# Kernel optimization log

Hardware: AMD Instinct MI355X
Metric: run time of the kernel (lower is better)

Reference implementation:

```python
import jax, jax.numpy as jnp
import numpy as np

E, TOPK = 8, 2
N_EMBD, TEXT_DIM, FULL = 1024, 1024, 1024
BS, SEQ = 8, 512

def setup_inputs() -> dict:
    key = jax.random.key(0)
    ks = jax.random.split(key, 8)
    return {
        "x": jax.random.normal(ks[0], (BS, SEQ, N_EMBD), jnp.float32),
        "dec_embeddings": jax.random.normal(ks[1], (BS, TEXT_DIM), jnp.float32),
        # router is zero-init in the module, but use small random weights so top-k is non-degenerate
        "router_w": jax.random.normal(ks[2], (E, TEXT_DIM), jnp.float32) * 0.02,
        "router_b": jnp.zeros((E,), jnp.float32),
        "w1": jax.random.normal(ks[3], (E, N_EMBD, N_EMBD), jnp.float32) * 0.02,
        "w2": jax.random.normal(ks[4], (E, N_EMBD, FULL), jnp.float32) * 0.02,
        "b1": jnp.zeros((E, 1, N_EMBD), jnp.float32),
        "b2": jnp.zeros((E, 1, FULL), jnp.float32),
    }

def reference(x, dec_embeddings, router_w, router_b, w1, w2, b1, b2):
    bs, seqlen, n_embd = x.shape
    logits = dec_embeddings @ router_w.T + router_b          # (bs, E)
    gate_probs = jax.nn.softmax(logits, axis=-1)
    topk_w, topk_idx = jax.lax.top_k(gate_probs, TOPK)       # (bs, k)
    topk_w = topk_w / jnp.sum(topk_w, axis=-1, keepdims=True)
    # dense all-expert 2-layer MLP (as written in the original)
    hidden = jax.nn.relu(jnp.einsum('bsn,enh->ebsh', x, w1) + b1[:, None])   # (E,bs,S,H)
    out_all = jnp.einsum('ebsh,ehf->ebsf', hidden, w2) + b2[:, None]          # (E,bs,S,F)
    out_b = jnp.transpose(out_all, (1, 0, 2, 3))             # (bs,E,S,F)
    # gather top-k expert outputs per batch item and combine
    sel = jnp.take_along_axis(out_b, topk_idx[:, :, None, None], axis=1)      # (bs,k,S,F)
    final_output = jnp.sum(topk_w[:, :, None, None] * sel, axis=1)            # (bs,S,F)
    combined_mask = jnp.max(jax.nn.one_hot(topk_idx, E, dtype=x.dtype), axis=1)  # (bs,E)
    aux_loss = E * jnp.sum(jnp.mean(gate_probs, axis=0) * jnp.mean(combined_mask, axis=0))
    return final_output, aux_loss, combined_mask, logits
```

## Files before the change

### kernel.cpp

```cpp
#include <hip/hip_runtime.h>
#include <hip/hip_bf16.h>
#include <stdint.h>

#define EXP 8
#define DIM 1024
#define SEQL 512
#define BATCH 8
#define OUT_FINAL_N (BATCH * SEQL * DIM)
#define OFF_AUX    4194304
#define OFF_MASK   4194305
#define OFF_LOGITS 4194369

typedef __bf16 bf16_t;
typedef bf16_t bf16x8 __attribute__((ext_vector_type(8)));
typedef bf16_t bf16x4 __attribute__((ext_vector_type(4)));
typedef float  f32x4  __attribute__((ext_vector_type(4)));

typedef __attribute__((address_space(1))) void* as1p;
typedef __attribute__((address_space(3))) void* as3p;

__device__ __forceinline__ void glds16(const void* g, void* l) {
  __builtin_amdgcn_global_load_lds((as1p)(void*)g, (as3p)l, 16, 0, 0);
}

__global__ __launch_bounds__(256) void prep_kernel(
    const float* __restrict__ x, const float* __restrict__ dec,
    const float* __restrict__ rw, const float* __restrict__ rb,
    const float* __restrict__ w1, const float* __restrict__ w2,
    bf16_t* __restrict__ xb, bf16_t* __restrict__ w1t, bf16_t* __restrict__ w2t,
    float* __restrict__ out_aux, float* __restrict__ out_mask,
    float* __restrict__ out_logits, int* __restrict__ idx_ws,
    float* __restrict__ w_ws) {
  __shared__ float tile[64][129];
  __shared__ float part[256];
  __shared__ float lg64[64];
  __shared__ float probs[64];
  __shared__ float msk[64];
  const int bid = blockIdx.x;
  const int t = threadIdx.x;

  if (bid < 2048) {
    const int z = bid >> 7;
    const int rem = bid & 127;
    const int k0 = (rem >> 4) * 128;
    const int n0 = (rem & 15) * 64;
    const float* src = (z < 8) ? (w1 + (size_t)z * DIM * DIM)
                               : (w2 + (size_t)(z - 8) * DIM * DIM);
    bf16_t* dst = (z < 8) ? (w1t + (size_t)z * DIM * DIM)
                          : (w2t + (size_t)(z - 8) * DIM * DIM);
    const int rr = t >> 4, c4 = t & 15;
    float4 v[8];
#pragma unroll
    for (int i = 0; i < 8; ++i)
      v[i] = *(const float4*)(src + (size_t)(k0 + rr + 16 * i) * DIM + n0 + c4 * 4);
#pragma unroll
    for (int i = 0; i < 8; ++i) {
      const int k = rr + 16 * i;
      tile[c4 * 4 + 0][k] = v[i].x;
      tile[c4 * 4 + 1][k] = v[i].y;
      tile[c4 * 4 + 2][k] = v[i].z;
      tile[c4 * 4 + 3][k] = v[i].w;
    }
    __syncthreads();
#pragma unroll
    for (int ii = 0; ii < 4; ++ii) {
      const int n = (t >> 4) + 16 * ii;
      const int c = t & 15;
      bf16x8 o;
#pragma unroll
      for (int wd = 0; wd < 8; ++wd) o[wd] = (bf16_t)tile[n][c * 8 + wd];
      *(bf16x8*)(dst + (size_t)(n0 + n) * DIM + k0 + c * 8) = o;
    }
  } else if (bid < 2048 + 512) {
    const int i0 = (bid - 2048) * 2048 + t;
    float4 v[8];
#pragma unroll
    for (int i = 0; i < 8; ++i) v[i] = ((const float4*)x)[i0 + i * 256];
#pragma unroll
    for (int i = 0; i < 8; ++i) {
      bf16x4 o;
      o[0] = (bf16_t)v[i].x; o[1] = (bf16_t)v[i].y;
      o[2] = (bf16_t)v[i].z; o[3] = (bf16_t)v[i].w;
      ((bf16x4*)xb)[i0 + i * 256] = o;
    }
  } else {
    const int p = t >> 2, seg = t & 3;
    const int b = p >> 3, e = p & 7;
    const float4* dv = (const float4*)(dec + b * DIM + seg * 256);
    const float4* wv = (const float4*)(rw + e * DIM + seg * 256);
    float s = 0.f;
#pragma unroll 8
    for (int i = 0; i < 64; ++i) {
      float4 a = dv[i], c = wv[i];
      s += a.x * c.x + a.y * c.y + a.z * c.z + a.w * c.w;
    }
    part[t] = s;
    __syncthreads();
    if (seg == 0) {
      float l = part[t] + part[t + 1] + part[t + 2] + part[t + 3] + rb[e];
      lg64[p] = l;
      out_logits[p] = l;
    }
    __syncthreads();
    if (t < 8) {
      float l[8];
      float mx = -1e30f;
#pragma unroll
      for (int k = 0; k < 8; ++k) { l[k] = lg64[t * 8 + k]; mx = fmaxf(mx, l[k]); }
      float pe[8];
      float sum = 0.f;
#pragma unroll
      for (int k = 0; k < 8; ++k) { pe[k] = expf(l[k] - mx); sum += pe[k]; }
      float inv = 1.f / sum;
#pragma unroll
      for (int k = 0; k < 8; ++k) { pe[k] *= inv; probs[t * 8 + k] = pe[k]; }
      int i0 = 0;
#pragma unroll
      for (int k = 1; k < 8; ++k) if (pe[k] > pe[i0]) i0 = k;
      int i1 = (i0 == 0) ? 1 : 0;
#pragma unroll
      for (int k = 0; k < 8; ++k) if (k != i0 && pe[k] > pe[i1]) i1 = k;
      float p0 = pe[i0], p1 = pe[i1];
      float invs = 1.f / (p0 + p1);
      idx_ws[t * 2] = i0;
      idx_ws[t * 2 + 1] = i1;
      w_ws[t * 2] = p0 * invs;
      w_ws[t * 2 + 1] = p1 * invs;
#pragma unroll
      for (int k = 0; k < 8; ++k) {
        float m = (k == i0 || k == i1) ? 1.f : 0.f;
        msk[t * 8 + k] = m;
        out_mask[t * 8 + k] = m;
      }
    }
    __syncthreads();
    if (t == 0) {
      float aux = 0.f;
#pragma unroll
      for (int k = 0; k < 8; ++k) {
        float mp = 0.f, mm = 0.f;
#pragma unroll
        for (int bb = 0; bb < 8; ++bb) { mp += probs[bb * 8 + k]; mm += msk[bb * 8 + k]; }
        aux += (mp * 0.125f) * (mm * 0.125f);
      }
      out_aux[0] = 8.f * aux;
    }
  }
}

__device__ __forceinline__ void kloop_64x128(const bf16_t* __restrict__ A,
                                             const bf16_t* __restrict__ Bt,
                                             char* sA, char* sB, int t,
                                             f32x4 acc[2][4]) {
  const int lane = t & 63;
  const int w = t >> 6, wr = w >> 1, wc = w & 1;
  const int m15 = lane & 15, q = lane >> 4;
  const int rl = t >> 2, cp = (t & 3) ^ (rl & 3);
  const bf16_t* ga  = A  + (size_t)rl * DIM + cp * 8;
  const bf16_t* gb0 = Bt + (size_t)rl * DIM + cp * 8;
  const bf16_t* gb1 = gb0 + (size_t)64 * DIM;

  const char* ra[2];
  const char* rb[4];
#pragma unroll
  for (int i = 0; i < 2; ++i) {
    const int r = wr * 32 + i * 16 + m15;
    ra[i] = sA + r * 64 + ((q ^ (r & 3)) * 16);
  }
#pragma unroll
  for (int j = 0; j < 4; ++j) {
    const int n = wc * 64 + j * 16 + m15;
    rb[j] = sB + n * 64 + ((q ^ (n & 3)) * 16);
  }

  glds16(ga,  sA + t * 16);
  glds16(gb0, sB + t * 16);
  glds16(gb1, sB + 4096 + t * 16);

  for (int kt = 0; kt < 32; ++kt) {
    const int cur = kt & 1;
    __syncthreads();
    if (kt < 31) {
      const int nxt = cur ^ 1;
      const int off = (kt + 1) * 32;
      glds16(ga + off,  sA + nxt * 4096 + t * 16);
      glds16(gb0 + off, sB + nxt * 8192 + t * 16);
      glds16(gb1 + off, sB + nxt * 8192 + 4096 + t * 16);
    }
    bf16x8 af[2], bfr[4];
#pragma unroll
    for (int i = 0; i < 2; ++i) af[i] = *(const bf16x8*)(ra[i] + cur * 4096);
#pragma unroll
    for (int j = 0; j < 4; ++j) bfr[j] = *(const bf16x8*)(rb[j] + cur * 8192);
#pragma unroll
    for (int i = 0; i < 2; ++i)
#pragma unroll
      for (int j = 0; j < 4; ++j)
        acc[i][j] = __builtin_amdgcn_mfma_f32_16x16x32_bf16(af[i], bfr[j], acc[i][j], 0, 0, 0);
  }
}

__global__ __launch_bounds__(256, 4) void gemm1_kernel(const bf16_t* __restrict__ xb,
                                                       const bf16_t* __restrict__ w1t,
                                                       const float* __restrict__ b1,
                                                       const int* __restrict__ topk_idx,
                                                       bf16_t* __restrict__ hidden) {
  __shared__ __align__(16) char smem[24576];
  const int tid = threadIdx.x;
  const int bN = blockIdx.x, bM = blockIdx.y, slot = blockIdx.z;
  const int b = slot >> 1;
  const int e = topk_idx[slot];

  const bf16_t* A  = xb + ((size_t)b * SEQL + bM * 64) * DIM;
  const bf16_t* Bt = w1t + ((size_t)e * DIM + bN * 128) * DIM;

  f32x4 acc[2][4];
#pragma unroll
  for (int i = 0; i < 2; ++i)
#pragma unroll
    for (int j = 0; j < 4; ++j) acc[i][j] = {0.f, 0.f, 0.f, 0.f};

  kloop_64x128(A, Bt, smem, smem + 8192, tid, acc);

  __syncthreads();
  bf16_t* hb = (bf16_t*)smem;
  const int lane = tid & 63, w = tid >> 6;
  const int wr = w >> 1, wc = w & 1;
  const int m15 = lane & 15, q = lane >> 4;
  const float* be = b1 + e * DIM;
#pragma unroll
  for (int i = 0; i < 2; ++i)
#pragma unroll
    for (int j = 0; j < 4; ++j) {
      const int colL = wc * 64 + j * 16 + m15;
      const float bias = be[bN * 128 + colL];
#pragma unroll
      for (int r = 0; r < 4; ++r) {
        const int rowL = wr * 32 + i * 16 + q * 4 + r;
        hb[rowL * 136 + colL] = (bf16_t)fmaxf(acc[i][j][r] + bias, 0.f);
      }
    }
  __syncthreads();
  bf16_t* H = hidden + (size_t)slot * SEQL * DIM + ((size_t)bM * 64) * DIM + bN * 128;
#pragma unroll
  for (int ii = 0; ii < 4; ++ii) {
    const int r = (tid >> 4) + 16 * ii;
    const int c = tid & 15;
    bf16x8 vv = *(const bf16x8*)(hb + r * 136 + c * 8);
    *(bf16x8*)(H + (size_t)r * DIM + c * 8) = vv;
  }
}

__global__ __launch_bounds__(512, 4) void gemm2_kernel(const bf16_t* __restrict__ hidden,
                                                       const bf16_t* __restrict__ w2t,
                                                       const float* __restrict__ b2,
                                                       const int* __restrict__ topk_idx,
                                                       const float* __restrict__ topk_w,
                                                       float* __restrict__ out) {
  __shared__ __align__(16) char smem[49152];
  const int tid = threadIdx.x;
  const int g = tid >> 8;
  const int t = tid & 255;
  const int bN = blockIdx.x, bM = blockIdx.y, b = blockIdx.z;
  const int e = topk_idx[b * 2 + g];
  const float sg = topk_w[b * 2 + g];

  char* sA = smem + g * 24576;
  char* sB = smem + g * 24576 + 8192;

  f32x4 acc[2][4];
#pragma unroll
  for (int i = 0; i < 2; ++i)
#pragma unroll
    for (int j = 0; j < 4; ++j) acc[i][j] = {0.f, 0.f, 0.f, 0.f};

  const bf16_t* A  = hidden + ((size_t)(b * 2 + g) * SEQL + bM * 64) * DIM;
  const bf16_t* Bt = w2t + ((size_t)e * DIM + bN * 128) * DIM;
  kloop_64x128(A, Bt, sA, sB, t, acc);

  __syncthreads();
  float* scr = (float*)smem;
  const int lane = t & 63, wv = t >> 6;
  const int wr = wv >> 1, wc = wv & 1;
  const int m15 = lane & 15, q = lane >> 4;
  const float w0 = topk_w[b * 2], w1v = topk_w[b * 2 + 1];
  const float* be0 = b2 + topk_idx[b * 2] * DIM;
  const float* be1 = b2 + topk_idx[b * 2 + 1] * DIM;
  float* O = out + (size_t)b * SEQL * DIM;

#pragma unroll
  for (int half = 0; half < 2; ++half) {
    if (g == 1) {
#pragma unroll
      for (int j = 0; j < 4; ++j)
#pragma unroll
        for (int r = 0; r < 4; ++r)
          scr[(j * 4 + r) * 256 + t] = sg * acc[half][j][r];
    }
    __syncthreads();
    if (g == 0) {
#pragma unroll
      for (int j = 0; j < 4; ++j) {
        const int col = bN * 128 + wc * 64 + j * 16 + m15;
        const float bb = w0 * be0[col] + w1v * be1[col];
        const int row = bM * 64 + wr * 32 + half * 16 + q * 4;
#pragma unroll
        for (int r = 0; r < 4; ++r)
          O[(size_t)(row + r) * DIM + col] =
              sg * acc[half][j][r] + scr[(j * 4 + r) * 256 + t] + bb;
      }
    }
    __syncthreads();
  }
}

extern "C" void kernel_launch(void* const* d_in, const int* in_sizes, int n_in,
                              void* d_out, int out_size, void* d_ws, size_t ws_size,
                              hipStream_t stream) {
  const float* x   = (const float*)d_in[0];
  const float* dec = (const float*)d_in[1];
  const float* rw  = (const float*)d_in[2];
  const float* rb  = (const float*)d_in[3];
  const float* w1  = (const float*)d_in[4];
  const float* w2  = (const float*)d_in[5];
  const float* b1  = (const float*)d_in[6];
  const float* b2  = (const float*)d_in[7];
  float* out = (float*)d_out;

  char* ws = (char*)d_ws;
  bf16_t* xb   = (bf16_t*)(ws);
  bf16_t* w1t  = (bf16_t*)(ws + (8u << 20));
  bf16_t* w2t  = (bf16_t*)(ws + (24u << 20));
  bf16_t* hid  = (bf16_t*)(ws + (40u << 20));
  int*    idxw = (int*)(ws + (56u << 20));
  float*  ww   = (float*)(ws + (56u << 20) + 64);

  hipLaunchKernelGGL(prep_kernel, dim3(2048 + 512 + 1), dim3(256), 0, stream,
                     x, dec, rw, rb, w1, w2, xb, w1t, w2t,
                     out + OFF_AUX, out + OFF_MASK, out + OFF_LOGITS, idxw, ww);
  hipLaunchKernelGGL(gemm1_kernel, dim3(8, 8, 16), dim3(256), 0, stream,
                     xb, w1t, b1, idxw, hid);
  hipLaunchKernelGGL(gemm2_kernel, dim3(8, 8, 8), dim3(512), 0, stream,
                     hid, w2t, b2, idxw, ww, out);
}
```

Before: 203.3 us.

## Overlap w2 transpose/convert with gemm1 by interleaving blocks in one kernel

Moves the fp32→bf16 transpose of w2 out of the prep kernel and into the gemm1 launch, interleaving transpose blocks (even ids) with gemm1 tile blocks (odd ids). The goal is to hide the memory-bound w2 conversion behind the compute-bound first GEMM and shorten the prep kernel. In exchange, gemm1 loses its launch_bounds occupancy hint of 4 and now uses a larger shared buffer sized for the transpose tile, which may reduce gemm1 occupancy.

```diff
diff --git a/kernel.cpp b/kernel.cpp
--- a/kernel.cpp
+++ b/kernel.cpp
@@ -23,56 +23,54 @@
   __builtin_amdgcn_global_load_lds((as1p)(void*)g, (as3p)l, 16, 0, 0);
 }
 
-__global__ __launch_bounds__(256) void prep_kernel(
+__device__ __forceinline__ void transpose_tile(const float* __restrict__ src,
+                                               bf16_t* __restrict__ dst,
+                                               int k0, int n0, int t,
+                                               char* smem_) {
+  float (*tile)[129] = (float (*)[129])smem_;
+  const int rr = t >> 4, c4 = t & 15;
+  float4 v[8];
+#pragma unroll
+  for (int i = 0; i < 8; ++i)
+    v[i] = *(const float4*)(src + (size_t)(k0 + rr + 16 * i) * DIM + n0 + c4 * 4);
+#pragma unroll
+  for (int i = 0; i < 8; ++i) {
+    const int k = rr + 16 * i;
+    tile[c4 * 4 + 0][k] = v[i].x;
+    tile[c4 * 4 + 1][k] = v[i].y;
+    tile[c4 * 4 + 2][k] = v[i].z;
+    tile[c4 * 4 + 3][k] = v[i].w;
+  }
+  __syncthreads();
+#pragma unroll
+  for (int ii = 0; ii < 4; ++ii) {
+    const int n = (t >> 4) + 16 * ii;
+    const int c = t & 15;
+    bf16x8 o;
+#pragma unroll
+    for (int wd = 0; wd < 8; ++wd) o[wd] = (bf16_t)tile[n][c * 8 + wd];
+    *(bf16x8*)(dst + (size_t)(n0 + n) * DIM + k0 + c * 8) = o;
+  }
+}
+
+__global__ __launch_bounds__(256) void k1_prep(
     const float* __restrict__ x, const float* __restrict__ dec,
     const float* __restrict__ rw, const float* __restrict__ rb,
-    const float* __restrict__ w1, const float* __restrict__ w2,
-    bf16_t* __restrict__ xb, bf16_t* __restrict__ w1t, bf16_t* __restrict__ w2t,
+    const float* __restrict__ w1,
+    bf16_t* __restrict__ xb, bf16_t* __restrict__ w1t,
     float* __restrict__ out_aux, float* __restrict__ out_mask,
     float* __restrict__ out_logits, int* __restrict__ idx_ws,
     float* __restrict__ w_ws) {
-  __shared__ float tile[64][129];
-  __shared__ float part[256];
-  __shared__ float lg64[64];
-  __shared__ float probs[64];
-  __shared__ float msk[64];
+  __shared__ __align__(16) char smem[33024];
   const int bid = blockIdx.x;
   const int t = threadIdx.x;
 
-  if (bid < 2048) {
-    const int z = bid >> 7;
-    const int rem = bid & 127;
-    const int k0 = (rem >> 4) * 128;
-    const int n0 = (rem & 15) * 64;
-    const float* src = (z < 8) ? (w1 + (size_t)z * DIM * DIM)
-                               : (w2 + (size_t)(z - 8) * DIM * DIM);
-    bf16_t* dst = (z < 8) ? (w1t + (size_t)z * DIM * DIM)
-                          : (w2t + (size_t)(z - 8) * DIM * DIM);
-    const int rr = t >> 4, c4 = t & 15;
-    float4 v[8];
-#pragma unroll
-    for (int i = 0; i < 8; ++i)
-      v[i] = *(const float4*)(src + (size_t)(k0 + rr + 16 * i) * DIM + n0 + c4 * 4);
-#pragma unroll
-    for (int i = 0; i < 8; ++i) {
-      const int k = rr + 16 * i;
-      tile[c4 * 4 + 0][k] = v[i].x;
-      tile[c4 * 4 + 1][k] = v[i].y;
-      tile[c4 * 4 + 2][k] = v[i].z;
-      tile[c4 * 4 + 3][k] = v[i].w;
-    }
-    __syncthreads();
-#pragma unroll
-    for (int ii = 0; ii < 4; ++ii) {
-      const int n = (t >> 4) + 16 * ii;
-      const int c = t & 15;
-      bf16x8 o;
-#pragma unroll
-      for (int wd = 0; wd < 8; ++wd) o[wd] = (bf16_t)tile[n][c * 8 + wd];
-      *(bf16x8*)(dst + (size_t)(n0 + n) * DIM + k0 + c * 8) = o;
-    }
-  } else if (bid < 2048 + 512) {
-    const int i0 = (bid - 2048) * 2048 + t;
+  if (bid < 1024) {
+    const int z = bid >> 7, rem = bid & 127;
+    transpose_tile(w1 + (size_t)z * DIM * DIM, w1t + (size_t)z * DIM * DIM,
+                   (rem >> 4) * 128, (rem & 15) * 64, t, smem);
+  } else if (bid < 1024 + 512) {
+    const int i0 = (bid - 1024) * 2048 + t;
     float4 v[8];
 #pragma unroll
     for (int i = 0; i < 8; ++i) v[i] = ((const float4*)x)[i0 + i * 256];
@@ -84,6 +82,10 @@
       ((bf16x4*)xb)[i0 + i * 256] = o;
     }
   } else {
+    float* part = (float*)smem;
+    float* lg64 = part + 256;
+    float* probs = lg64 + 64;
+    float* msk = probs + 64;
     const int p = t >> 2, seg = t & 3;
     const int b = p >> 3, e = p & 7;
     const float4* dv = (const float4*)(dec + b * DIM + seg * 256);
@@ -200,14 +202,25 @@
   }
 }
 
-__global__ __launch_bounds__(256, 4) void gemm1_kernel(const bf16_t* __restrict__ xb,
-                                                       const bf16_t* __restrict__ w1t,
-                                                       const float* __restrict__ b1,
-                                                       const int* __restrict__ topk_idx,
-                                                       bf16_t* __restrict__ hidden) {
-  __shared__ __align__(16) char smem[24576];
+__global__ __launch_bounds__(256) void k2_w2t_gemm1(
+    const float* __restrict__ w2, bf16_t* __restrict__ w2t,
+    const bf16_t* __restrict__ xb, const bf16_t* __restrict__ w1t,
+    const float* __restrict__ b1, const int* __restrict__ topk_idx,
+    bf16_t* __restrict__ hidden) {
+  __shared__ __align__(16) char smem[33024];
+  const int bid = blockIdx.x;
   const int tid = threadIdx.x;
-  const int bN = blockIdx.x, bM = blockIdx.y, slot = blockIdx.z;
+
+  if ((bid & 1) == 0) {
+    const int ti = bid >> 1;
+    const int z = ti >> 7, rem = ti & 127;
+    transpose_tile(w2 + (size_t)z * DIM * DIM, w2t + (size_t)z * DIM * DIM,
+                   (rem >> 4) * 128, (rem & 15) * 64, tid, smem);
+    return;
+  }
+
+  const int g = bid >> 1;
+  const int bN = g & 7, bM = (g >> 3) & 7, slot = g >> 6;
   const int b = slot >> 1;
   const int e = topk_idx[slot];
 
@@ -335,11 +348,11 @@
   int*    idxw = (int*)(ws + (56u << 20));
   float*  ww   = (float*)(ws + (56u << 20) + 64);
 
-  hipLaunchKernelGGL(prep_kernel, dim3(2048 + 512 + 1), dim3(256), 0, stream,
-                     x, dec, rw, rb, w1, w2, xb, w1t, w2t,
+  hipLaunchKernelGGL(k1_prep, dim3(1024 + 512 + 1), dim3(256), 0, stream,
+                     x, dec, rw, rb, w1, xb, w1t,
                      out + OFF_AUX, out + OFF_MASK, out + OFF_LOGITS, idxw, ww);
-  hipLaunchKernelGGL(gemm1_kernel, dim3(8, 8, 16), dim3(256), 0, stream,
-                     xb, w1t, b1, idxw, hid);
+  hipLaunchKernelGGL(k2_w2t_gemm1, dim3(2048), dim3(256), 0, stream,
+                     w2, w2t, xb, w1t, b1, idxw, hid);
   hipLaunchKernelGGL(gemm2_kernel, dim3(8, 8, 8), dim3(512), 0, stream,
                      hid, w2t, b2, idxw, ww, out);
 }
```

Result: slower. 221.2 us (+8.8%).

## Fold gate weight into gemm1 and accumulate both experts in one gemm2 block

Applied to the files above, without the earlier changes.

Gemm1 now scales the ReLU hidden activations by the top-k gate weight. Gemm2 can then run both experts' K-loops back to back in one 256-thread block into a single accumulator, instead of two 256-thread groups combined through shared memory. The epilogue stages the tile in padded LDS and writes coalesced float4 stores with the bias precomputed. This halves gemm2's shared memory and threads per block and removes the cross-group reduction. The cost is a serial K-loop twice as long per block and bf16 rounding of the gate-scaled hidden values.

```diff
diff --git a/kernel.cpp b/kernel.cpp
--- a/kernel.cpp
+++ b/kernel.cpp
@@ -6,7 +6,6 @@
 #define DIM 1024
 #define SEQL 512
 #define BATCH 8
-#define OUT_FINAL_N (BATCH * SEQL * DIM)
 #define OFF_AUX    4194304
 #define OFF_MASK   4194305
 #define OFF_LOGITS 4194369
@@ -200,16 +199,18 @@
   }
 }
 
-__global__ __launch_bounds__(256, 4) void gemm1_kernel(const bf16_t* __restrict__ xb,
-                                                       const bf16_t* __restrict__ w1t,
-                                                       const float* __restrict__ b1,
-                                                       const int* __restrict__ topk_idx,
-                                                       bf16_t* __restrict__ hidden) {
+__global__ __launch_bounds__(256) void gemm1_kernel(const bf16_t* __restrict__ xb,
+                                                    const bf16_t* __restrict__ w1t,
+                                                    const float* __restrict__ b1,
+                                                    const int* __restrict__ topk_idx,
+                                                    const float* __restrict__ topk_w,
+                                                    bf16_t* __restrict__ hidden) {
   __shared__ __align__(16) char smem[24576];
   const int tid = threadIdx.x;
   const int bN = blockIdx.x, bM = blockIdx.y, slot = blockIdx.z;
   const int b = slot >> 1;
   const int e = topk_idx[slot];
+  const float gw = topk_w[slot];
 
   const bf16_t* A  = xb + ((size_t)b * SEQL + bM * 64) * DIM;
   const bf16_t* Bt = w1t + ((size_t)e * DIM + bN * 128) * DIM;
@@ -237,7 +238,7 @@
 #pragma unroll
       for (int r = 0; r < 4; ++r) {
         const int rowL = wr * 32 + i * 16 + q * 4 + r;
-        hb[rowL * 136 + colL] = (bf16_t)fmaxf(acc[i][j][r] + bias, 0.f);
+        hb[rowL * 136 + colL] = (bf16_t)(gw * fmaxf(acc[i][j][r] + bias, 0.f));
       }
     }
   __syncthreads();
@@ -251,22 +252,17 @@
   }
 }
 
-__global__ __launch_bounds__(512, 4) void gemm2_kernel(const bf16_t* __restrict__ hidden,
-                                                       const bf16_t* __restrict__ w2t,
-                                                       const float* __restrict__ b2,
-                                                       const int* __restrict__ topk_idx,
-                                                       const float* __restrict__ topk_w,
-                                                       float* __restrict__ out) {
-  __shared__ __align__(16) char smem[49152];
+__global__ __launch_bounds__(256) void gemm2_kernel(const bf16_t* __restrict__ hidden,
+                                                    const bf16_t* __restrict__ w2t,
+                                                    const float* __restrict__ b2,
+                                                    const int* __restrict__ topk_idx,
+                                                    const float* __restrict__ topk_w,
+                                                    float* __restrict__ out) {
+  __shared__ __align__(16) char smem[24576];
   const int tid = threadIdx.x;
-  const int g = tid >> 8;
-  const int t = tid & 255;
   const int bN = blockIdx.x, bM = blockIdx.y, b = blockIdx.z;
-  const int e = topk_idx[b * 2 + g];
-  const float sg = topk_w[b * 2 + g];
-
-  char* sA = smem + g * 24576;
-  char* sB = smem + g * 24576 + 8192;
+  const int e0 = topk_idx[b * 2], e1 = topk_idx[b * 2 + 1];
+  const float w0 = topk_w[b * 2], w1v = topk_w[b * 2 + 1];
 
   f32x4 acc[2][4];
 #pragma unroll
@@ -274,41 +270,48 @@
 #pragma unroll
     for (int j = 0; j < 4; ++j) acc[i][j] = {0.f, 0.f, 0.f, 0.f};
 
-  const bf16_t* A  = hidden + ((size_t)(b * 2 + g) * SEQL + bM * 64) * DIM;
-  const bf16_t* Bt = w2t + ((size_t)e * DIM + bN * 128) * DIM;
-  kloop_64x128(A, Bt, sA, sB, t, acc);
+  const bf16_t* A0 = hidden + ((size_t)(b * 2) * SEQL + bM * 64) * DIM;
+  const bf16_t* B0 = w2t + ((size_t)e0 * DIM + bN * 128) * DIM;
+  kloop_64x128(A0, B0, smem, smem + 8192, tid, acc);
+
+  const bf16_t* A1 = hidden + ((size_t)(b * 2 + 1) * SEQL + bM * 64) * DIM;
+  const bf16_t* B1 = w2t + ((size_t)e1 * DIM + bN * 128) * DIM;
+  kloop_64x128(A1, B1, smem, smem + 8192, tid, acc);
 
   __syncthreads();
   float* scr = (float*)smem;
-  const int lane = t & 63, wv = t >> 6;
-  const int wr = wv >> 1, wc = wv & 1;
+  const int lane = tid & 63, w = tid >> 6;
+  const int wr = w >> 1, wc = w & 1;
   const int m15 = lane & 15, q = lane >> 4;
-  const float w0 = topk_w[b * 2], w1v = topk_w[b * 2 + 1];
-  const float* be0 = b2 + topk_idx[b * 2] * DIM;
-  const float* be1 = b2 + topk_idx[b * 2 + 1] * DIM;
+  const float* be0 = b2 + e0 * DIM;
+  const float* be1 = b2 + e1 * DIM;
+  float bb[4];
+#pragma unroll
+  for (int j = 0; j < 4; ++j) {
+    const int col = bN * 128 + wc * 64 + j * 16 + m15;
+    bb[j] = w0 * be0[col] + w1v * be1[col];
+  }
   float* O = out + (size_t)b * SEQL * DIM;
 
 #pragma unroll
   for (int half = 0; half < 2; ++half) {
-    if (g == 1) {
-#pragma unroll
-      for (int j = 0; j < 4; ++j)
-#pragma unroll
-        for (int r = 0; r < 4; ++r)
-          scr[(j * 4 + r) * 256 + t] = sg * acc[half][j][r];
-    }
-    __syncthreads();
-    if (g == 0) {
-#pragma unroll
-      for (int j = 0; j < 4; ++j) {
-        const int col = bN * 128 + wc * 64 + j * 16 + m15;
-        const float bb = w0 * be0[col] + w1v * be1[col];
-        const int row = bM * 64 + wr * 32 + half * 16 + q * 4;
-#pragma unroll
-        for (int r = 0; r < 4; ++r)
-          O[(size_t)(row + r) * DIM + col] =
-              sg * acc[half][j][r] + scr[(j * 4 + r) * 256 + t] + bb;
+#pragma unroll
+    for (int j = 0; j < 4; ++j) {
+      const int colL = wc * 64 + j * 16 + m15;
+#pragma unroll
+      for (int r = 0; r < 4; ++r) {
+        const int lrow = wr * 16 + q * 4 + r;
+        scr[lrow * 132 + colL] = acc[half][j][r] + bb[j];
       }
+    }
+    __syncthreads();
+#pragma unroll
+    for (int ii = 0; ii < 4; ++ii) {
+      const int lrow = tid >> 3;
+      const int cch = (tid & 7) + 8 * ii;
+      const float4 v4 = *(const float4*)(scr + lrow * 132 + cch * 4);
+      const int grow = bM * 64 + half * 16 + (lrow < 16 ? lrow : lrow + 16);
+      *(float4*)(O + (size_t)grow * DIM + bN * 128 + cch * 4) = v4;
     }
     __syncthreads();
   }
@@ -339,7 +342,7 @@
                      x, dec, rw, rb, w1, w2, xb, w1t, w2t,
                      out + OFF_AUX, out + OFF_MASK, out + OFF_LOGITS, idxw, ww);
   hipLaunchKernelGGL(gemm1_kernel, dim3(8, 8, 16), dim3(256), 0, stream,
-                     xb, w1t, b1, idxw, hid);
-  hipLaunchKernelGGL(gemm2_kernel, dim3(8, 8, 8), dim3(512), 0, stream,
+                     xb, w1t, b1, idxw, ww, hid);
+  hipLaunchKernelGGL(gemm2_kernel, dim3(8, 8, 8), dim3(256), 0, stream,
                      hid, w2t, b2, idxw, ww, out);
 }
```

Result: slower. 207.6 us (+2.1%).
